# Kernel optimization log

Measured on AMD Instinct MI355X. Metric: run time of the kernel, lower is better.

The kernel has to match this reference:

```python
import jax, jax.numpy as jnp
import numpy as np

HOPS = 3  # max_hops; C has HOPS+1 tables

def setup_inputs() -> dict:
    key = jax.random.key(0)
    k1, k2, k3 = jax.random.split(key, 3)
    B, M, S, V, D = 32, 512, 10, 32000, 128
    story = jax.random.randint(k1, (B, M, S), 0, V)
    hidden = jax.random.normal(k2, (B, 1, D), dtype=jnp.float32)
    # hop+1 embedding tables, initialized N(0, 0.1) like the torch module
    C = 0.1 * jax.random.normal(k3, (HOPS + 1, V, D), dtype=jnp.float32)
    return {"story": story, "hidden": hidden, "C": C}

def reference(story, hidden, C):
    # story: [B, M, S] int tokens; hidden: [B, 1, D]; C: [HOPS+1, V, D]
    u = jnp.squeeze(hidden, axis=1)  # [B, D]
    prob_logit = None
    for h in range(HOPS):
        # embedding gather + bag-sum over sentence dim -> [B, M, D]
        embed_A = jnp.take(C[h], story, axis=0).sum(axis=2)
        # dot-product attention logits against current query u
        prob_logit = jnp.einsum('bmd,bd->bm', embed_A, u)  # [B, M]
        prob = jax.nn.softmax(prob_logit, axis=1)
        # second table gather + bag-sum, then softmax-weighted combine
        embed_C = jnp.take(C[h + 1], story, axis=0).sum(axis=2)  # [B, M, D]
        o_k = jnp.einsum('bm,bmd->bd', prob, embed_C)  # [B, D]
        u = u + o_k
    return prob_logit, u
```

## Files before the change

kernel.cpp:

```cpp
#include <hip/hip_runtime.h>

#define BB 32
#define MM 512
#define SS 10
#define VV 32000
#define DD 128
#define HOPS 3
#define BM (BB * MM)
#define NCHUNK 32
#define CHM (MM / NCHUNK)
#define PSTRIDE 132


__global__ __launch_bounds__(256) void precompute_E12(const int* __restrict__ story,
                                                      const float* __restrict__ C,
                                                      float* __restrict__ E) {
    const int wid = (blockIdx.x * 256 + threadIdx.x) >> 6;
    const int lane = threadIdx.x & 63;
    const int t = blockIdx.y + 1;
    const int* st = story + (size_t)wid * SS;
    int tok[SS];
#pragma unroll
    for (int s = 0; s < SS; ++s) tok[s] = st[s];
    const float* Ct = C + (size_t)t * VV * DD;
    float ax = 0.f, ay = 0.f;
#pragma unroll
    for (int s = 0; s < SS; ++s) {
        const float2 v = ((const float2*)(Ct + (size_t)tok[s] * DD))[lane];
        ax += v.x; ay += v.y;
    }
    ((float2*)(E + ((size_t)(t - 1) * BM + wid) * DD))[lane] = make_float2(ax, ay);
}

template <int HOP>
__global__ __launch_bounds__(256) void hop_fused(const int* __restrict__ story,
                                                 const float* __restrict__ Cg,
                                                 const float* __restrict__ Elog,
                                                 const float* __restrict__ Eout,
                                                 const float* __restrict__ uprev,
                                                 const float* __restrict__ pin,
                                                 float* __restrict__ uwrite,
                                                 float* __restrict__ logit,
                                                 float* __restrict__ pout) {
    const int b = blockIdx.y, c = blockIdx.x;
    const int tid = threadIdx.x;
    const int w = tid >> 6, lane = tid & 63;

    __shared__ float su[DD];
    if (tid < DD) {
        float v = uprev[b * DD + tid];
        if (HOP > 0) {
            float num = 0.f, den = 0.f;
            for (int cc = 0; cc < NCHUNK; ++cc) {
                const float* p = pin + ((size_t)b * NCHUNK + cc) * PSTRIDE;
                num += p[tid];
                den += p[DD];
            }
            v += num / den;
            if (c == 0) uwrite[b * DD + tid] = v;
        }
        su[tid] = v;
    }
    __syncthreads();
    const float2 uv = ((const float2*)su)[lane];

    float nx = 0.f, ny = 0.f, den = 0.f;
    for (int k = 0; k < CHM / 4; ++k) {
        const int m = c * CHM + k * 4 + w;
        const int bm = b * MM + m;
        float ex, ey;
        if (HOP == 0) {
            const int* st = story + (size_t)bm * SS;
            int tok[SS];
#pragma unroll
            for (int s = 0; s < SS; ++s) tok[s] = st[s];
            ex = 0.f; ey = 0.f;
#pragma unroll
            for (int s = 0; s < SS; ++s) {
                const float2 v = ((const float2*)(Cg + (size_t)tok[s] * DD))[lane];
                ex += v.x; ey += v.y;
            }
        } else {
            const float2 v = ((const float2*)(Elog + (size_t)bm * DD))[lane];
            ex = v.x; ey = v.y;
        }
        float l = ex * uv.x + ey * uv.y;
#pragma unroll
        for (int off = 32; off; off >>= 1) l += __shfl_xor(l, off, 64);
        if (HOP == 2 && lane == 0) logit[bm] = l;
        const float e = expf(l);
        float ox, oy;
        if (HOP == 2) {
            const int* st = story + (size_t)bm * SS;
            int tok[SS];
#pragma unroll
            for (int s = 0; s < SS; ++s) tok[s] = st[s];
            ox = 0.f; oy = 0.f;
#pragma unroll
            for (int s = 0; s < SS; ++s) {
                const float2 v = ((const float2*)(Cg + (size_t)tok[s] * DD))[lane];
                ox += v.x; oy += v.y;
            }
        } else {
            const float2 v = ((const float2*)(Eout + (size_t)bm * DD))[lane];
            ox = v.x; oy = v.y;
        }
        nx += e * ox; ny += e * oy; den += e;
    }

    __shared__ float rx[4][64], ry[4][64], rd[4];
    rx[w][lane] = nx; ry[w][lane] = ny;
    if (lane == 0) rd[w] = den;
    __syncthreads();
    if (w == 0) {
        const float sx = rx[0][lane] + rx[1][lane] + rx[2][lane] + rx[3][lane];
        const float sy = ry[0][lane] + ry[1][lane] + ry[2][lane] + ry[3][lane];
        float* prow = pout + ((size_t)b * NCHUNK + c) * PSTRIDE;
        ((float2*)prow)[lane] = make_float2(sx, sy);
        if (lane == 0) prow[DD] = rd[0] + rd[1] + rd[2] + rd[3];
    }
}

__global__ __launch_bounds__(128) void final_u(const float* __restrict__ pin,
                                               const float* __restrict__ u2,
                                               float* __restrict__ uout) {
    const int b = blockIdx.x, d = threadIdx.x;
    float num = 0.f, den = 0.f;
    for (int cc = 0; cc < NCHUNK; ++cc) {
        const float* p = pin + ((size_t)b * NCHUNK + cc) * PSTRIDE;
        num += p[d];
        den += p[DD];
    }
    uout[b * DD + d] = u2[b * DD + d] + num / den;
}

__global__ __launch_bounds__(256) void init_u(const float* __restrict__ hidden,
                                              float* __restrict__ u) {
    int i = blockIdx.x * 256 + threadIdx.x;
    if (i < BB * DD) u[i] = hidden[i];
}

__global__ __launch_bounds__(256) void logit_kernel(const int* __restrict__ story,
                                                    const float* __restrict__ Ch,
                                                    const float* __restrict__ u,
                                                    float* __restrict__ logit) {
    int wid = (blockIdx.x * 256 + threadIdx.x) >> 6;
    int lane = threadIdx.x & 63;
    if (wid >= BB * MM) return;
    int b = wid >> 9;
    const int* st = story + (size_t)wid * SS;
    int tok[SS];
#pragma unroll
    for (int s = 0; s < SS; ++s) tok[s] = st[s];
    float ax = 0.f, ay = 0.f;
#pragma unroll
    for (int s = 0; s < SS; ++s) {
        const float2 v = ((const float2*)(Ch + (size_t)tok[s] * DD))[lane];
        ax += v.x; ay += v.y;
    }
    const float2 uv = ((const float2*)(u + b * DD))[lane];
    float p = ax * uv.x + ay * uv.y;
#pragma unroll
    for (int off = 32; off; off >>= 1) p += __shfl_down(p, off, 64);
    if (lane == 0) logit[wid] = p;
}

__global__ __launch_bounds__(256) void softmax_kernel(const float* __restrict__ logit,
                                                      float* __restrict__ prob) {
    int b = blockIdx.x;
    int t = threadIdx.x;
    __shared__ float red[8];
    float l0 = logit[b * MM + t];
    float l1 = logit[b * MM + 256 + t];
    float mx = fmaxf(l0, l1);
#pragma unroll
    for (int off = 32; off; off >>= 1) mx = fmaxf(mx, __shfl_xor(mx, off, 64));
    if ((t & 63) == 0) red[t >> 6] = mx;
    __syncthreads();
    mx = fmaxf(fmaxf(red[0], red[1]), fmaxf(red[2], red[3]));
    float e0 = expf(l0 - mx), e1 = expf(l1 - mx);
    float s = e0 + e1;
#pragma unroll
    for (int off = 32; off; off >>= 1) s += __shfl_xor(s, off, 64);
    if ((t & 63) == 0) red[4 + (t >> 6)] = s;
    __syncthreads();
    s = red[4] + red[5] + red[6] + red[7];
    float inv = 1.0f / s;
    prob[b * MM + t] = e0 * inv;
    prob[b * MM + 256 + t] = e1 * inv;
}

__global__ __launch_bounds__(256) void partial_kernel(const int* __restrict__ story,
                                                      const float* __restrict__ Ch1,
                                                      const float* __restrict__ prob,
                                                      float* __restrict__ partial,
                                                      int chunk) {
    int b = blockIdx.y, c = blockIdx.x;
    int w = threadIdx.x >> 6, lane = threadIdx.x & 63;
    int m0 = c * chunk;
    float ax = 0.f, ay = 0.f;
    for (int m = m0 + w; m < m0 + chunk; m += 4) {
        float pw = prob[b * MM + m];
        const int* st = story + (size_t)(b * MM + m) * SS;
        int tok[SS];
#pragma unroll
        for (int s = 0; s < SS; ++s) tok[s] = st[s];
        float sx = 0.f, sy = 0.f;
#pragma unroll
        for (int s = 0; s < SS; ++s) {
            const float2 v = ((const float2*)(Ch1 + (size_t)tok[s] * DD))[lane];
            sx += v.x; sy += v.y;
        }
        ax += pw * sx; ay += pw * sy;
    }
    __shared__ float redx[4][64];
    __shared__ float redy[4][64];
    redx[w][lane] = ax;
    redy[w][lane] = ay;
    __syncthreads();
    if (w == 0) {
        float ox = redx[0][lane] + redx[1][lane] + redx[2][lane] + redx[3][lane];
        float oy = redy[0][lane] + redy[1][lane] + redy[2][lane] + redy[3][lane];
        float2* dst = (float2*)(partial + ((size_t)b * gridDim.x + c) * DD);
        dst[lane] = make_float2(ox, oy);
    }
}

__global__ __launch_bounds__(256) void update_kernel(const float* __restrict__ partial,
                                                     float* __restrict__ u, int NC) {
    int i = blockIdx.x * 256 + threadIdx.x;
    if (i >= BB * DD) return;
    int b = i >> 7, d = i & 127;
    float s = 0.f;
    for (int c = 0; c < NC; ++c) s += partial[((size_t)b * NC + c) * DD + d];
    u[i] += s;
}

extern "C" void kernel_launch(void* const* d_in, const int* in_sizes, int n_in,
                              void* d_out, int out_size, void* d_ws, size_t ws_size,
                              hipStream_t stream) {
    const int*   story  = (const int*)d_in[0];
    const float* hidden = (const float*)d_in[1];
    const float* Cmat   = (const float*)d_in[2];

    float* out   = (float*)d_out;
    float* logit = out;
    float* u     = out + BB * MM;

    const size_t szE = (size_t)2 * BM * DD;
    const size_t szP = (size_t)BB * NCHUNK * PSTRIDE;
    const size_t need = (szE + 2 * szP + 2 * BB * DD) * sizeof(float);

    if (ws_size >= need) {
        float* E  = (float*)d_ws;
        float* E1 = E;
        float* E2 = E + (size_t)BM * DD;
        float* Pa = E + szE;
        float* Pb = Pa + szP;
        float* u1 = Pb + szP;
        float* u2 = u1 + BB * DD;
        const float* C0 = Cmat;
        const float* C3 = Cmat + (size_t)3 * VV * DD;

        precompute_E12<<<dim3(BM / 4, 2), 256, 0, stream>>>(story, Cmat, E);
        hop_fused<0><<<dim3(NCHUNK, BB), 256, 0, stream>>>(
            story, C0, nullptr, E1, hidden, nullptr, nullptr, nullptr, Pa);
        hop_fused<1><<<dim3(NCHUNK, BB), 256, 0, stream>>>(
            story, nullptr, E1, E2, hidden, Pa, u1, nullptr, Pb);
        hop_fused<2><<<dim3(NCHUNK, BB), 256, 0, stream>>>(
            story, C3, E2, nullptr, u1, Pb, u2, logit, Pa);
        final_u<<<BB, 128, 0, stream>>>(Pa, u2, u);
    } else {
        float* prob = (float*)d_ws;
        int NC = 32;
        while (NC > 1 && (size_t)(BB * MM + BB * NC * DD) * 4 > ws_size) NC >>= 1;
        float* partial = prob + BB * MM;
        int chunk = MM / NC;

        init_u<<<(BB * DD + 255) / 256, 256, 0, stream>>>(hidden, u);
        for (int h = 0; h < HOPS; ++h) {
            const float* Ca = Cmat + (size_t)h * VV * DD;
            const float* Cc = Cmat + (size_t)(h + 1) * VV * DD;
            logit_kernel<<<(BB * MM) / 4, 256, 0, stream>>>(story, Ca, u, logit);
            softmax_kernel<<<BB, 256, 0, stream>>>(logit, prob);
            partial_kernel<<<dim3(NC, BB), 256, 0, stream>>>(story, Cc, prob, partial, chunk);
            update_kernel<<<(BB * DD + 255) / 256, 256, 0, stream>>>(partial, u, NC);
        }
    }
}
```

Measured before the change: 67.04 us.

## Convert embedding tables to bf16 each call and fuse E precompute into hops

Adds a kernel that converts all four fp32 embedding tables to packed bf16 on every call, and has each hop gather bf16 rows, which halves the bytes per token gather. The separate precompute of E1/E2 is removed: each hop now gathers its output table itself and writes the bag sum for the next hop's logits. The per-call conversion reads the full 65 MB of tables and writes 33 MB, which may cost more than the gather traffic it saves. bf16 rounding of the tables also lowers accuracy.

```diff
diff --git a/kernel.cpp b/kernel.cpp
--- a/kernel.cpp
+++ b/kernel.cpp
@@ -11,37 +11,43 @@
 #define CHM (MM / NCHUNK)
 #define PSTRIDE 132
 
-
-__global__ __launch_bounds__(256) void precompute_E12(const int* __restrict__ story,
-                                                      const float* __restrict__ C,
-                                                      float* __restrict__ E) {
-    const int wid = (blockIdx.x * 256 + threadIdx.x) >> 6;
-    const int lane = threadIdx.x & 63;
-    const int t = blockIdx.y + 1;
-    const int* st = story + (size_t)wid * SS;
-    int tok[SS];
-#pragma unroll
-    for (int s = 0; s < SS; ++s) tok[s] = st[s];
-    const float* Ct = C + (size_t)t * VV * DD;
-    float ax = 0.f, ay = 0.f;
-#pragma unroll
-    for (int s = 0; s < SS; ++s) {
-        const float2 v = ((const float2*)(Ct + (size_t)tok[s] * DD))[lane];
-        ax += v.x; ay += v.y;
-    }
-    ((float2*)(E + ((size_t)(t - 1) * BM + wid) * DD))[lane] = make_float2(ax, ay);
+__device__ __forceinline__ unsigned bfrn(float f) {
+    unsigned u = __float_as_uint(f);
+    return (u + 0x7FFFu + ((u >> 16) & 1u)) >> 16;
+}
+__device__ __forceinline__ float bflo(unsigned q) {
+    return __uint_as_float(q << 16);
+}
+__device__ __forceinline__ float bfhi(unsigned q) {
+    return __uint_as_float(q & 0xFFFF0000u);
+}
+
+
+__global__ __launch_bounds__(256) void cvt_bf16(const float* __restrict__ C,
+                                                unsigned* __restrict__ Cb ) {
+    const int gid = blockIdx.x * 256 + threadIdx.x;
+    const float4 f0 = ((const float4*)C)[gid * 2];
+    const float4 f1 = ((const float4*)C)[gid * 2 + 1];
+    uint4 o;
+    o.x = bfrn(f0.x) | (bfrn(f0.y) << 16);
+    o.y = bfrn(f0.z) | (bfrn(f0.w) << 16);
+    o.z = bfrn(f1.x) | (bfrn(f1.y) << 16);
+    o.w = bfrn(f1.z) | (bfrn(f1.w) << 16);
+    ((uint4*)Cb)[gid] = o;
 }
 
 template <int HOP>
-__global__ __launch_bounds__(256) void hop_fused(const int* __restrict__ story,
-                                                 const float* __restrict__ Cg,
-                                                 const float* __restrict__ Elog,
-                                                 const float* __restrict__ Eout,
-                                                 const float* __restrict__ uprev,
-                                                 const float* __restrict__ pin,
-                                                 float* __restrict__ uwrite,
-                                                 float* __restrict__ logit,
-                                                 float* __restrict__ pout) {
+__global__ __launch_bounds__(256) void hop_k(const int* __restrict__ story,
+                                             const unsigned* __restrict__ Clog,
+                                             const unsigned* __restrict__ Cout,
+                                             const float* __restrict__ Elog,
+                                             float* __restrict__ Eout,
+                                             const float* __restrict__ uprev,
+                                             const float* __restrict__ pin,
+                                             const float* __restrict__ den_in_unused,
+                                             float* __restrict__ uwrite,
+                                             float* __restrict__ logit,
+                                             float* __restrict__ pout) {
     const int b = blockIdx.y, c = blockIdx.x;
     const int tid = threadIdx.x;
     const int w = tid >> 6, lane = tid & 63;
@@ -50,13 +56,13 @@
     if (tid < DD) {
         float v = uprev[b * DD + tid];
         if (HOP > 0) {
-            float num = 0.f, den = 0.f;
+            float num = 0.f, dsum = 0.f;
             for (int cc = 0; cc < NCHUNK; ++cc) {
                 const float* p = pin + ((size_t)b * NCHUNK + cc) * PSTRIDE;
                 num += p[tid];
-                den += p[DD];
+                dsum += p[DD];
             }
-            v += num / den;
+            v += num / dsum;
             if (c == 0) uwrite[b * DD + tid] = v;
         }
         su[tid] = v;
@@ -65,20 +71,22 @@
     const float2 uv = ((const float2*)su)[lane];
 
     float nx = 0.f, ny = 0.f, den = 0.f;
+#pragma unroll
     for (int k = 0; k < CHM / 4; ++k) {
         const int m = c * CHM + k * 4 + w;
         const int bm = b * MM + m;
+        int tok[SS];
+        const int* st = story + (size_t)bm * SS;
+#pragma unroll
+        for (int s = 0; s < SS; ++s) tok[s] = st[s];
+
         float ex, ey;
         if (HOP == 0) {
-            const int* st = story + (size_t)bm * SS;
-            int tok[SS];
-#pragma unroll
-            for (int s = 0; s < SS; ++s) tok[s] = st[s];
             ex = 0.f; ey = 0.f;
 #pragma unroll
             for (int s = 0; s < SS; ++s) {
-                const float2 v = ((const float2*)(Cg + (size_t)tok[s] * DD))[lane];
-                ex += v.x; ey += v.y;
+                const unsigned q = (Clog + (size_t)tok[s] * (DD / 2))[lane];
+                ex += bflo(q); ey += bfhi(q);
             }
         } else {
             const float2 v = ((const float2*)(Elog + (size_t)bm * DD))[lane];
@@ -89,35 +97,28 @@
         for (int off = 32; off; off >>= 1) l += __shfl_xor(l, off, 64);
         if (HOP == 2 && lane == 0) logit[bm] = l;
         const float e = expf(l);
-        float ox, oy;
-        if (HOP == 2) {
-            const int* st = story + (size_t)bm * SS;
-            int tok[SS];
-#pragma unroll
-            for (int s = 0; s < SS; ++s) tok[s] = st[s];
-            ox = 0.f; oy = 0.f;
-#pragma unroll
-            for (int s = 0; s < SS; ++s) {
-                const float2 v = ((const float2*)(Cg + (size_t)tok[s] * DD))[lane];
-                ox += v.x; oy += v.y;
-            }
-        } else {
-            const float2 v = ((const float2*)(Eout + (size_t)bm * DD))[lane];
-            ox = v.x; oy = v.y;
-        }
-        nx += e * ox; ny += e * oy; den += e;
-    }
-
-    __shared__ float rx[4][64], ry[4][64], rd[4];
-    rx[w][lane] = nx; ry[w][lane] = ny;
-    if (lane == 0) rd[w] = den;
+
+        float rx = 0.f, ry = 0.f;
+#pragma unroll
+        for (int s = 0; s < SS; ++s) {
+            const unsigned q = (Cout + (size_t)tok[s] * (DD / 2))[lane];
+            rx += bflo(q); ry += bfhi(q);
+        }
+        if (HOP < 2)
+            ((float2*)(Eout + (size_t)bm * DD))[lane] = make_float2(rx, ry);
+        nx += e * rx; ny += e * ry; den += e;
+    }
+
+    __shared__ float sx[4][64], sy[4][64], sd[4];
+    sx[w][lane] = nx; sy[w][lane] = ny;
+    if (lane == 0) sd[w] = den;
     __syncthreads();
     if (w == 0) {
-        const float sx = rx[0][lane] + rx[1][lane] + rx[2][lane] + rx[3][lane];
-        const float sy = ry[0][lane] + ry[1][lane] + ry[2][lane] + ry[3][lane];
+        const float ox = sx[0][lane] + sx[1][lane] + sx[2][lane] + sx[3][lane];
+        const float oy = sy[0][lane] + sy[1][lane] + sy[2][lane] + sy[3][lane];
         float* prow = pout + ((size_t)b * NCHUNK + c) * PSTRIDE;
-        ((float2*)prow)[lane] = make_float2(sx, sy);
-        if (lane == 0) prow[DD] = rd[0] + rd[1] + rd[2] + rd[3];
+        ((float2*)prow)[lane] = make_float2(ox, oy);
+        if (lane == 0) prow[DD] = sd[0] + sd[1] + sd[2] + sd[3];
     }
 }
 
@@ -245,31 +246,37 @@
 
     float* out   = (float*)d_out;
     float* logit = out;
-    float* u     = out + BB * MM;
-
-    const size_t szE = (size_t)2 * BM * DD;
-    const size_t szP = (size_t)BB * NCHUNK * PSTRIDE;
-    const size_t need = (szE + 2 * szP + 2 * BB * DD) * sizeof(float);
+    float* uout  = out + BB * MM;
+
+    const size_t szCb = (size_t)4 * VV * DD / 2;
+    const size_t szE  = (size_t)BM * DD;
+    const size_t szP  = (size_t)BB * NCHUNK * PSTRIDE;
+    const size_t need = (szCb + 2 * szE + 3 * szP + 2 * BB * DD) * sizeof(float);
 
     if (ws_size >= need) {
-        float* E  = (float*)d_ws;
-        float* E1 = E;
-        float* E2 = E + (size_t)BM * DD;
-        float* Pa = E + szE;
-        float* Pb = Pa + szP;
-        float* u1 = Pb + szP;
+        unsigned* Cb = (unsigned*)d_ws;
+        float* E1 = (float*)d_ws + szCb;
+        float* E2 = E1 + szE;
+        float* P0 = E2 + szE;
+        float* P1 = P0 + szP;
+        float* P2 = P1 + szP;
+        float* u1 = P2 + szP;
         float* u2 = u1 + BB * DD;
-        const float* C0 = Cmat;
-        const float* C3 = Cmat + (size_t)3 * VV * DD;
-
-        precompute_E12<<<dim3(BM / 4, 2), 256, 0, stream>>>(story, Cmat, E);
-        hop_fused<0><<<dim3(NCHUNK, BB), 256, 0, stream>>>(
-            story, C0, nullptr, E1, hidden, nullptr, nullptr, nullptr, Pa);
-        hop_fused<1><<<dim3(NCHUNK, BB), 256, 0, stream>>>(
-            story, nullptr, E1, E2, hidden, Pa, u1, nullptr, Pb);
-        hop_fused<2><<<dim3(NCHUNK, BB), 256, 0, stream>>>(
-            story, C3, E2, nullptr, u1, Pb, u2, logit, Pa);
-        final_u<<<BB, 128, 0, stream>>>(Pa, u2, u);
+
+        const unsigned* C0b = Cb;
+        const unsigned* C1b = Cb + (size_t)1 * VV * DD / 2;
+        const unsigned* C2b = Cb + (size_t)2 * VV * DD / 2;
+        const unsigned* C3b = Cb + (size_t)3 * VV * DD / 2;
+
+        cvt_bf16<<<(4 * VV * DD / 8) / 256, 256, 0, stream>>>(Cmat, Cb);
+
+        hop_k<0><<<dim3(NCHUNK, BB), 256, 0, stream>>>(
+            story, C0b, C1b, nullptr, E1, hidden, nullptr, nullptr, nullptr, nullptr, P0);
+        hop_k<1><<<dim3(NCHUNK, BB), 256, 0, stream>>>(
+            story, nullptr, C2b, E1, E2, hidden, P0, nullptr, u1, nullptr, P1);
+        hop_k<2><<<dim3(NCHUNK, BB), 256, 0, stream>>>(
+            story, nullptr, C3b, E2, nullptr, u1, P1, nullptr, u2, logit, P2);
+        final_u<<<BB, 128, 0, stream>>>(P2, u2, uout);
     } else {
         float* prob = (float*)d_ws;
         int NC = 32;
@@ -277,14 +284,14 @@
         float* partial = prob + BB * MM;
         int chunk = MM / NC;
 
-        init_u<<<(BB * DD + 255) / 256, 256, 0, stream>>>(hidden, u);
+        init_u<<<(BB * DD + 255) / 256, 256, 0, stream>>>(hidden, uout);
         for (int h = 0; h < HOPS; ++h) {
             const float* Ca = Cmat + (size_t)h * VV * DD;
             const float* Cc = Cmat + (size_t)(h + 1) * VV * DD;
-            logit_kernel<<<(BB * MM) / 4, 256, 0, stream>>>(story, Ca, u, logit);
+            logit_kernel<<<(BB * MM) / 4, 256, 0, stream>>>(story, Ca, uout, logit);
             softmax_kernel<<<BB, 256, 0, stream>>>(logit, prob);
             partial_kernel<<<dim3(NC, BB), 256, 0, stream>>>(story, Cc, prob, partial, chunk);
-            update_kernel<<<(BB * DD + 255) / 256, 256, 0, stream>>>(partial, u, NC);
-        }
-    }
-}
+            update_kernel<<<(BB * DD + 255) / 256, 256, 0, stream>>>(partial, uout, NC);
+        }
+    }
+}
```

Measured after the change: 66.10 us. No clear change (-1.4%).
